# Kernel tuning notes

Hardware: AMD Instinct MI355X
Metric: run time of the kernel (lower is better)

## Reference

```python
import jax, jax.numpy as jnp
import numpy as np

B, T, D = 1, 2048, 3072
N, K, H = 16, 8, 256  # heads, kv heads, head dim
SOFT_CAP = 50.0
WINDOW = 1024
ROPE_BASE = 10000.0
ROPE_SCALE = 1.0
K_MASK = -2.3819763e+38
EPS = 1e-6


def rms_norm(x, scale=None):
    var = jnp.mean(jnp.square(x), axis=-1, keepdims=True)
    y = x * jax.lax.rsqrt(var + EPS)
    if scale is not None:
        y = y * (1.0 + scale)
    return y


def apply_rope(x, positions):
    # x: [B, T, n, H], positions: [B, T] int
    half = x.shape[-1] // 2
    fraction = 2.0 * jnp.arange(half, dtype=jnp.float32) / x.shape[-1]
    timescale = ROPE_BASE ** fraction  # [half]
    sinusoid = positions[..., None].astype(jnp.float32) / timescale  # [B,T,half]
    sinusoid = sinusoid[..., None, :] / ROPE_SCALE  # [B,T,1,half]
    sin, cos = jnp.sin(sinusoid), jnp.cos(sinusoid)
    first, second = jnp.split(x, 2, axis=-1)
    out = jnp.concatenate([first * cos - second * sin,
                           second * cos + first * sin], axis=-1)
    return out.astype(x.dtype)


def setup_inputs() -> dict:
    key = jax.random.key(0)
    ks = jax.random.split(key, 6)
    x = jax.random.normal(ks[0], (B, T, D), jnp.float32)
    segment_pos = jnp.broadcast_to(jnp.arange(T, dtype=jnp.int32), (B, T))
    attn_mask = jnp.broadcast_to(jnp.tril(jnp.ones((T, T), bool)), (B, T, T))
    w_q = jax.random.normal(ks[1], (N, D, H), jnp.float32) * 0.02
    w_kv = jax.random.normal(ks[2], (2, K, D, H), jnp.float32) * 0.02
    w_out = jax.random.normal(ks[3], (N, H, D), jnp.float32) * 0.02
    q_scale = jax.random.normal(ks[4], (H,), jnp.float32) * 0.1
    k_scale = jax.random.normal(ks[5], (H,), jnp.float32) * 0.1
    return {"x": x, "segment_pos": segment_pos, "attn_mask": attn_mask,
            "w_q": w_q, "w_kv": w_kv, "w_out": w_out,
            "q_scale": q_scale, "k_scale": k_scale}


def reference(x, segment_pos, attn_mask, w_q, w_kv, w_out, q_scale, k_scale):
    # Q projection + QK-RMSNorm + RoPE
    q = jnp.einsum('BTD,NDH->BTNH', x, w_q)
    q = rms_norm(q, q_scale)
    q = apply_rope(q, segment_pos)
    # fused KV projection
    kv = jnp.einsum('BSD,CKDH->CBSKH', x, w_kv)
    k_proj, v_proj = kv[0], kv[1]
    k_proj = rms_norm(k_proj, k_scale)
    v_proj = rms_norm(v_proj)  # value norm has no scale
    k_proj = apply_rope(k_proj, segment_pos)
    # GQA logits: q [B,T,K,G,H] x k [B,S,K,H]
    G = N // K
    qg = q.reshape(B, T, K, G, H)
    logits = jnp.einsum('BTKGH,BSKH->BTKGS', qg, k_proj).reshape(B, T, N, T)
    # logit soft-capping
    logits = jnp.tanh(logits / SOFT_CAP) * SOFT_CAP
    # sliding-window mask (cache_positions == segment_pos since cache is None)
    pos_q = segment_pos[:, :, None]
    pos_k = segment_pos[:, None, :]
    sliding = (pos_k > pos_q - WINDOW) & (pos_k < pos_q + WINDOW)  # [B,T,S]
    mask = attn_mask & sliding
    padded = jnp.where(mask[:, :, None, :], logits, K_MASK)
    probs = jax.nn.softmax(padded, axis=-1).astype(k_proj.dtype)
    enc = jnp.einsum('BTKGS,BSKH->BTKGH',
                     probs.reshape(B, T, K, G, T), v_proj).reshape(B, T, N, H)
    attn_output = jnp.einsum('BTNH,NHD->BTD', enc, w_out)
    return attn_output
```

## Files before the change

kernel.cpp:

```cpp
#include <hip/hip_runtime.h>
#include <math.h>

#define T_SEQ 2048
#define D_MODEL 3072
#define NQ 16
#define NKV 8
#define HD 256
#define NHEADS_TOT 32
#define QKV_COLS 8192
#define SOFT_CAP 50.0f
#define WINDOW 1024
#define K_MASK -2.3819763e38f

typedef __attribute__((ext_vector_type(8))) short bf16x8;
typedef __attribute__((ext_vector_type(4))) float f32x4;

__device__ __forceinline__ unsigned short f2bf(float f) {
    union { float f; unsigned u; } v; v.f = f;
    unsigned r = (v.u + 0x7fff + ((v.u >> 16) & 1)) >> 16;
    return (unsigned short)r;
}
__device__ __forceinline__ float bf2f(unsigned short u) {
    union { unsigned u; float f; } v; v.u = ((unsigned)u) << 16;
    return v.f;
}

__device__ __forceinline__ void gl_lds16(const unsigned short* g, unsigned short* l) {
    __builtin_amdgcn_global_load_lds(
        (const __attribute__((address_space(1))) void*)g,
        (__attribute__((address_space(3))) void*)l, 16, 0, 0);
}

__global__ __launch_bounds__(256) void k_convert(const float* __restrict__ src,
                                                 unsigned short* __restrict__ dst, int n4) {
    int i = blockIdx.x * 256 + threadIdx.x;
    if (i >= n4) return;
    float4 v = ((const float4*)src)[i];
    ushort4 o;
    o.x = f2bf(v.x); o.y = f2bf(v.y); o.z = f2bf(v.z); o.w = f2bf(v.w);
    ((ushort4*)dst)[i] = o;
}

__global__ __launch_bounds__(256) void k_transpose_bf16(const float* __restrict__ src,
                                                        unsigned short* __restrict__ dst,
                                                        int R, int C) {
    __shared__ float tile[32][33];
    int b = blockIdx.z;
    src += (size_t)b * R * C;
    dst += (size_t)b * R * C;
    int c0 = blockIdx.x * 32, r0 = blockIdx.y * 32;
    int tx = threadIdx.x, ty = threadIdx.y;
    #pragma unroll
    for (int i = ty; i < 32; i += 8)
        tile[i][tx] = src[(size_t)(r0 + i) * C + c0 + tx];
    __syncthreads();
    #pragma unroll
    for (int i = ty; i < 32; i += 8)
        dst[(size_t)(c0 + i) * R + r0 + tx] = f2bf(tile[tx][i]);
}

__global__ __launch_bounds__(256) void k_transpose_v(const unsigned short* __restrict__ src,
                                                     unsigned short* __restrict__ dst) {
    __shared__ unsigned short tile[32][34];
    int kk = blockIdx.z;
    src += (size_t)kk * T_SEQ * HD;
    dst += (size_t)kk * HD * T_SEQ;
    int h0 = blockIdx.x * 32, t0 = blockIdx.y * 32;
    int tx = threadIdx.x, ty = threadIdx.y;
    #pragma unroll
    for (int i = ty; i < 32; i += 8)
        tile[i][tx] = src[(size_t)(t0 + i) * HD + h0 + tx];
    __syncthreads();
    #pragma unroll
    for (int i = ty; i < 32; i += 8)
        dst[(size_t)(h0 + i) * T_SEQ + t0 + tx] = tile[tx][i];
}

__global__ __launch_bounds__(128) void k_trig(const int* __restrict__ spos,
                                              float2* __restrict__ tbl) {
    int t = blockIdx.x, hh = threadIdx.x;
    float fr = (float)hh * (1.0f / 128.0f);
    float ts = __expf(fr * 9.210340371976184f);
    float ang = (float)spos[t] / ts;
    float2 sc;
    sc.x = __sinf(ang);
    sc.y = __cosf(ang);
    tbl[(size_t)t * 128 + hh] = sc;
}

template <int OUT_BF16>
__global__ __launch_bounds__(256) void k_gemm_nt(const unsigned short* __restrict__ A,
                                                 const unsigned short* __restrict__ BT,
                                                 void* __restrict__ Cout,
                                                 int M, int N, int Kd) {
    __shared__ unsigned short As[128 * 64];
    __shared__ unsigned short Bs[128 * 64];
    const int tid = threadIdx.x;
    const int wave = tid >> 6, lane = tid & 63;
    const int col = lane & 15, quad = lane >> 4;
    const int wr = wave >> 1, wc = wave & 1;

    const int gx = M >> 7;
    int p = blockIdx.x;
    int xcd = p & 7, q = p >> 3;
    int i_t = q % gx, jj = q / gx;
    int j_t = jj * 8 + xcd;
    const int m0 = i_t * 128, n0 = j_t * 128;

    const int sub = wave & 1, isB = wave >> 1;
    const unsigned short* srcBase = isB ? (BT + (size_t)(n0 + sub * 64) * Kd)
                                        : (A + (size_t)(m0 + sub * 64) * Kd);
    unsigned short* ldsBase = (isB ? Bs : As) + sub * 64 * 64;
    const int lrow = lane >> 3, lchk = lane & 7;
    int soff[8];
    #pragma unroll
    for (int s = 0; s < 8; s++) {
        int r = s * 8 + lrow;
        soff[s] = r * Kd + ((lchk ^ (r & 7)) * 8);
    }

    f32x4 acc[4][4];
    #pragma unroll
    for (int i = 0; i < 4; i++)
        #pragma unroll
        for (int j = 0; j < 4; j++)
            acc[i][j] = (f32x4){0.f, 0.f, 0.f, 0.f};

    const int sw = col & 7;

    for (int k0 = 0; k0 < Kd; k0 += 64) {
        #pragma unroll
        for (int s = 0; s < 8; s++)
            gl_lds16(srcBase + soff[s] + k0, ldsBase + s * 512);
        __syncthreads();

        #pragma unroll
        for (int kk = 0; kk < 2; kk++) {
            bf16x8 af[4], bfr[4];
            const int chko = ((kk * 4 + quad) ^ sw) * 8;
            #pragma unroll
            for (int i = 0; i < 4; i++)
                af[i] = *(const bf16x8*)&As[(wr * 64 + i * 16 + col) * 64 + chko];
            #pragma unroll
            for (int j = 0; j < 4; j++)
                bfr[j] = *(const bf16x8*)&Bs[(wc * 64 + j * 16 + col) * 64 + chko];
            #pragma unroll
            for (int i = 0; i < 4; i++)
                #pragma unroll
                for (int j = 0; j < 4; j++)
                    acc[i][j] = __builtin_amdgcn_mfma_f32_16x16x32_bf16(af[i], bfr[j], acc[i][j], 0, 0, 0);
        }
        __syncthreads();
    }

    #pragma unroll
    for (int i = 0; i < 4; i++) {
        int row = m0 + wr * 64 + i * 16 + quad * 4;
        #pragma unroll
        for (int j = 0; j < 4; j++) {
            int c = n0 + wc * 64 + j * 16 + col;
            #pragma unroll
            for (int r = 0; r < 4; r++) {
                float v = acc[i][j][r];
                if (OUT_BF16)
                    ((unsigned short*)Cout)[(size_t)(row + r) * N + c] = f2bf(v);
                else
                    ((float*)Cout)[(size_t)(row + r) * N + c] = v;
            }
        }
    }
}

__global__ __launch_bounds__(256) void k_norm_rope(const unsigned short* __restrict__ qkv,
                                                   const float2* __restrict__ trig,
                                                   const float* __restrict__ qscale,
                                                   const float* __restrict__ kscale,
                                                   unsigned short* __restrict__ qh,
                                                   unsigned short* __restrict__ kh,
                                                   unsigned short* __restrict__ vh) {
    const int t = blockIdx.x, slot = blockIdx.y, h = threadIdx.x;
    float val = bf2f(qkv[(size_t)t * QKV_COLS + slot * HD + h]);
    float ss = val * val;
    #pragma unroll
    for (int m = 1; m < 64; m <<= 1) ss += __shfl_xor(ss, m, 64);
    __shared__ float wsum[4];
    __shared__ float ybuf[256];
    if ((h & 63) == 0) wsum[h >> 6] = ss;
    __syncthreads();
    float tot = wsum[0] + wsum[1] + wsum[2] + wsum[3];
    float y = val * rsqrtf(tot * (1.0f / 256.0f) + 1e-6f);
    if (slot < 16) y *= (1.0f + qscale[h]);
    else if (slot < 24) y *= (1.0f + kscale[h]);

    if (slot < 24) {
        ybuf[h] = y;
        __syncthreads();
        int hh = h & 127;
        float2 sc = trig[(size_t)t * 128 + hh];
        float sn = sc.x, cs = sc.y;
        float other = ybuf[(h < 128) ? (h + 128) : (h - 128)];
        float outv = (h < 128) ? (y * cs - other * sn) : (y * cs + other * sn);
        if (slot < 16)
            qh[((size_t)slot * T_SEQ + t) * HD + h] = f2bf(outv);
        else
            kh[((size_t)(slot - 16) * T_SEQ + t) * HD + h] = f2bf(outv);
    } else {
        vh[((size_t)(slot - 24) * T_SEQ + t) * HD + h] = f2bf(y);
    }
}

__global__ __launch_bounds__(256) void k_attn(const unsigned short* __restrict__ qh,
                                              const unsigned short* __restrict__ kh,
                                              const unsigned short* __restrict__ vT,
                                              unsigned short* __restrict__ enc) {
    __shared__ unsigned short Ks[32 * 256];
    __shared__ unsigned short Vs[256 * 32];
    __shared__ unsigned short Pl[4][16 * 40];

    const int tid = threadIdx.x;
    const int wave = tid >> 6, lane = tid & 63;
    const int col = lane & 15, quad = lane >> 4;
    const int kk = blockIdx.x;
    const int t0b = blockIdx.y * 32;
    const int headSel = wave & 1, rowSel = wave >> 1;
    const int n = kk * 2 + headSel;
    const int tw = t0b + rowSel * 16;

    const unsigned short* qp = qh + ((size_t)n * T_SEQ + tw) * HD;
    const unsigned short* kp = kh + (size_t)kk * T_SEQ * HD;
    const unsigned short* vp = vT + (size_t)kk * HD * T_SEQ;

    bf16x8 qf[8];
    #pragma unroll
    for (int c = 0; c < 8; c++)
        qf[c] = *(const bf16x8*)(qp + (size_t)col * HD + c * 32 + quad * 8);

    int preK[4], preV[4], ldsKo[4], ldsVo[4];
    #pragma unroll
    for (int i = 0; i < 4; i++) {
        int krow = 2 * (wave * 4 + i) + (lane >> 5);
        int kpos = lane & 31;
        preK[i] = krow * HD + ((kpos ^ (krow & 7)) * 8);
        ldsKo[i] = (wave * 4 + i) * 512;
        int vh2 = (wave * 4 + i) * 16 + (lane >> 2);
        int vpp = lane & 3;
        preV[i] = vh2 * T_SEQ + ((vpp ^ (vh2 & 3)) * 8);
        ldsVo[i] = (wave * 4 + i) * 512;
    }

    f32x4 o[16];
    #pragma unroll
    for (int h = 0; h < 16; h++) o[h] = (f32x4){0.f, 0.f, 0.f, 0.f};
    float lsum[4] = {0.f, 0.f, 0.f, 0.f};

    int s_begin = t0b - (WINDOW - 1);
    if (s_begin < 0) s_begin = 0;
    s_begin &= ~31;
    const int s_end = t0b + 32;

    for (int s0 = s_begin; s0 < s_end; s0 += 32) {
        #pragma unroll
        for (int i = 0; i < 4; i++)
            gl_lds16(kp + (size_t)s0 * HD + preK[i], &Ks[ldsKo[i]]);
        #pragma unroll
        for (int i = 0; i < 4; i++)
            gl_lds16(vp + (size_t)s0 + preV[i], &Vs[ldsVo[i]]);
        __syncthreads();

        f32x4 S0 = (f32x4){0.f, 0.f, 0.f, 0.f};
        f32x4 S1 = (f32x4){0.f, 0.f, 0.f, 0.f};
        #pragma unroll
        for (int c = 0; c < 8; c++) {
            bf16x8 kf = *(const bf16x8*)&Ks[(size_t)col * HD + (((c * 4 + quad) ^ (col & 7)) * 8)];
            S0 = __builtin_amdgcn_mfma_f32_16x16x32_bf16(qf[c], kf, S0, 0, 0, 0);
        }
        #pragma unroll
        for (int c = 0; c < 8; c++) {
            bf16x8 kf = *(const bf16x8*)&Ks[(size_t)(16 + col) * HD + (((c * 4 + quad) ^ (col & 7)) * 8)];
            S1 = __builtin_amdgcn_mfma_f32_16x16x32_bf16(qf[c], kf, S1, 0, 0, 0);
        }

        #pragma unroll
        for (int r = 0; r < 4; r++) {
            int t = tw + quad * 4 + r;
            int sA = s0 + col, sB = sA + 16;
            bool vA = (sA <= t) && (sA >= t - (WINDOW - 1));
            bool vB = (sB <= t) && (sB >= t - (WINDOW - 1));
            float eA = __expf(S0[r] * (2.0f / SOFT_CAP));
            float eB = __expf(S1[r] * (2.0f / SOFT_CAP));
            float rA = __builtin_amdgcn_rcpf(eA + 1.0f);
            float rB = __builtin_amdgcn_rcpf(eB + 1.0f);
            float pA = __expf(SOFT_CAP - 2.0f * SOFT_CAP * rA);
            float pB = __expf(SOFT_CAP - 2.0f * SOFT_CAP * rB);
            pA = vA ? pA : 0.0f;
            pB = vB ? pB : 0.0f;
            lsum[r] += pA + pB;
            Pl[wave][(quad * 4 + r) * 40 + col] = f2bf(pA);
            Pl[wave][(quad * 4 + r) * 40 + 16 + col] = f2bf(pB);
        }

        bf16x8 pf = *(const bf16x8*)&Pl[wave][col * 40 + quad * 8];

        #pragma unroll
        for (int ht = 0; ht < 16; ht++) {
            int h = ht * 16 + col;
            bf16x8 vf = *(const bf16x8*)&Vs[(size_t)h * 32 + ((quad ^ (h & 3)) * 8)];
            o[ht] = __builtin_amdgcn_mfma_f32_16x16x32_bf16(pf, vf, o[ht], 0, 0, 0);
        }
        __syncthreads();
    }

    #pragma unroll
    for (int r = 0; r < 4; r++) {
        #pragma unroll
        for (int m = 1; m < 16; m <<= 1)
            lsum[r] += __shfl_xor(lsum[r], m, 16);
        lsum[r] = 1.0f / lsum[r];
    }
    #pragma unroll
    for (int ht = 0; ht < 16; ht++) {
        #pragma unroll
        for (int r = 0; r < 4; r++) {
            int t = tw + quad * 4 + r;
            enc[(size_t)t * (NQ * HD) + n * HD + ht * 16 + col] = f2bf(o[ht][r] * lsum[r]);
        }
    }
}

extern "C" void kernel_launch(void* const* d_in, const int* in_sizes, int n_in,
                              void* d_out, int out_size, void* d_ws, size_t ws_size,
                              hipStream_t stream) {
    const float* x       = (const float*)d_in[0];
    const int*   spos    = (const int*)d_in[1];
    const float* w_q     = (const float*)d_in[3];
    const float* w_kv    = (const float*)d_in[4];
    const float* w_out   = (const float*)d_in[5];
    const float* q_scale = (const float*)d_in[6];
    const float* k_scale = (const float*)d_in[7];
    float* out = (float*)d_out;

    char* ws = (char*)d_ws;
    unsigned short* xb     = (unsigned short*)(ws + 0);
    unsigned short* vh     = (unsigned short*)(ws + 0);
    float2*         trig   = (float2*)(ws + 8388608);
    unsigned short* wT     = (unsigned short*)(ws + 12582912);
    unsigned short* wToutb = (unsigned short*)(ws + 12582912);
    unsigned short* encb   = (unsigned short*)(ws + 37748736);
    unsigned short* qkv    = (unsigned short*)(ws + 62914560);
    unsigned short* qh     = (unsigned short*)(ws + 96468992);
    unsigned short* kh     = (unsigned short*)(ws + 113246208);
    unsigned short* vT     = (unsigned short*)(ws + 121634816);

    k_convert<<<dim3((T_SEQ * D_MODEL / 4 + 255) / 256), dim3(256), 0, stream>>>(
        x, xb, T_SEQ * D_MODEL / 4);
    k_transpose_bf16<<<dim3(HD / 32, D_MODEL / 32, NQ), dim3(32, 8), 0, stream>>>(
        w_q, wT, D_MODEL, HD);
    k_transpose_bf16<<<dim3(HD / 32, D_MODEL / 32, 16), dim3(32, 8), 0, stream>>>(
        w_kv, wT + (size_t)4096 * D_MODEL, D_MODEL, HD);
    k_gemm_nt<1><<<dim3((T_SEQ / 128) * (QKV_COLS / 128)), dim3(256), 0, stream>>>(
        xb, wT, qkv, T_SEQ, QKV_COLS, D_MODEL);
    k_trig<<<dim3(T_SEQ), dim3(128), 0, stream>>>(spos, trig);
    k_transpose_bf16<<<dim3(D_MODEL / 32, 4096 / 32, 1), dim3(32, 8), 0, stream>>>(
        w_out, wToutb, 4096, D_MODEL);
    k_norm_rope<<<dim3(T_SEQ, NHEADS_TOT), dim3(256), 0, stream>>>(
        qkv, trig, q_scale, k_scale, qh, kh, vh);
    k_transpose_v<<<dim3(HD / 32, T_SEQ / 32, NKV), dim3(32, 8), 0, stream>>>(vh, vT);
    k_attn<<<dim3(NKV, T_SEQ / 32), dim3(256), 0, stream>>>(qh, kh, vT, encb);
    k_gemm_nt<0><<<dim3((T_SEQ / 128) * (D_MODEL / 128)), dim3(256), 0, stream>>>(
        encb, wToutb, out, T_SEQ, D_MODEL, NQ * HD);
}
```

Measured before the change: 550.2 us.

## Use 128x64-tile GEMM for output projection and batch four heads per norm-rope block

```diff
diff --git a/kernel.cpp b/kernel.cpp
--- a/kernel.cpp
+++ b/kernel.cpp
@@ -171,6 +171,88 @@
     }
 }
 
+__global__ __launch_bounds__(256) void k_gemm2(const unsigned short* __restrict__ A,
+                                               const unsigned short* __restrict__ BT,
+                                               float* __restrict__ C,
+                                               int M, int N, int Kd) {
+    __shared__ unsigned short As[128 * 64];
+    __shared__ unsigned short Bs[64 * 64];
+    const int tid = threadIdx.x;
+    const int wave = tid >> 6, lane = tid & 63;
+    const int col = lane & 15, quad = lane >> 4;
+
+    const int gx = M >> 7;
+    int p = blockIdx.x;
+    int xcd = p & 7, q = p >> 3;
+    int i_t = q % gx, jj = q / gx;
+    int j_t = jj * 8 + xcd;
+    const int m0 = i_t * 128, n0 = j_t * 64;
+
+    const int lrow = lane >> 3, lchk = lane & 7;
+    int soffA[4], soffB[2];
+    #pragma unroll
+    for (int s = 0; s < 4; s++) {
+        int r = (wave * 4 + s) * 8 + lrow;
+        soffA[s] = r * Kd + ((lchk ^ (r & 7)) * 8);
+    }
+    #pragma unroll
+    for (int s = 0; s < 2; s++) {
+        int r = (wave * 2 + s) * 8 + lrow;
+        soffB[s] = r * Kd + ((lchk ^ (r & 7)) * 8);
+    }
+    const unsigned short* Ab = A + (size_t)m0 * Kd;
+    const unsigned short* Bb = BT + (size_t)n0 * Kd;
+
+    f32x4 acc[2][4];
+    #pragma unroll
+    for (int i = 0; i < 2; i++)
+        #pragma unroll
+        for (int j = 0; j < 4; j++)
+            acc[i][j] = (f32x4){0.f, 0.f, 0.f, 0.f};
+
+    const int sw = col & 7;
+
+    for (int k0 = 0; k0 < Kd; k0 += 64) {
+        #pragma unroll
+        for (int s = 0; s < 4; s++)
+            gl_lds16(Ab + soffA[s] + k0, &As[(wave * 4 + s) * 512]);
+        #pragma unroll
+        for (int s = 0; s < 2; s++)
+            gl_lds16(Bb + soffB[s] + k0, &Bs[(wave * 2 + s) * 512]);
+        __syncthreads();
+
+        #pragma unroll
+        for (int kk = 0; kk < 2; kk++) {
+            const int chko = ((kk * 4 + quad) ^ sw) * 8;
+            bf16x8 af[2], bfr[4];
+            #pragma unroll
+            for (int i = 0; i < 2; i++)
+                af[i] = *(const bf16x8*)&As[(wave * 32 + i * 16 + col) * 64 + chko];
+            #pragma unroll
+            for (int j = 0; j < 4; j++)
+                bfr[j] = *(const bf16x8*)&Bs[(j * 16 + col) * 64 + chko];
+            #pragma unroll
+            for (int i = 0; i < 2; i++)
+                #pragma unroll
+                for (int j = 0; j < 4; j++)
+                    acc[i][j] = __builtin_amdgcn_mfma_f32_16x16x32_bf16(af[i], bfr[j], acc[i][j], 0, 0, 0);
+        }
+        __syncthreads();
+    }
+
+    #pragma unroll
+    for (int i = 0; i < 2; i++) {
+        int row = m0 + wave * 32 + i * 16 + quad * 4;
+        #pragma unroll
+        for (int j = 0; j < 4; j++) {
+            int c = n0 + j * 16 + col;
+            #pragma unroll
+            for (int r = 0; r < 4; r++)
+                C[(size_t)(row + r) * N + c] = acc[i][j][r];
+        }
+    }
+}
+
 __global__ __launch_bounds__(256) void k_norm_rope(const unsigned short* __restrict__ qkv,
                                                    const float2* __restrict__ trig,
                                                    const float* __restrict__ qscale,
@@ -178,35 +260,56 @@
                                                    unsigned short* __restrict__ qh,
                                                    unsigned short* __restrict__ kh,
                                                    unsigned short* __restrict__ vh) {
-    const int t = blockIdx.x, slot = blockIdx.y, h = threadIdx.x;
-    float val = bf2f(qkv[(size_t)t * QKV_COLS + slot * HD + h]);
-    float ss = val * val;
-    #pragma unroll
-    for (int m = 1; m < 64; m <<= 1) ss += __shfl_xor(ss, m, 64);
-    __shared__ float wsum[4];
-    __shared__ float ybuf[256];
-    if ((h & 63) == 0) wsum[h >> 6] = ss;
+    const int t = blockIdx.x, y = blockIdx.y, h = threadIdx.x;
+    __shared__ float wsum[4][4];
+    __shared__ float ybuf[3][256];
+
+    float val[4];
+    #pragma unroll
+    for (int g = 0; g < 4; g++)
+        val[g] = bf2f(qkv[(size_t)t * QKV_COLS + (y + g * 8) * HD + h]);
+
+    float ssg[4];
+    #pragma unroll
+    for (int g = 0; g < 4; g++) {
+        float ss = val[g] * val[g];
+        #pragma unroll
+        for (int m = 1; m < 64; m <<= 1) ss += __shfl_xor(ss, m, 64);
+        ssg[g] = ss;
+    }
+    if ((h & 63) == 0) {
+        #pragma unroll
+        for (int g = 0; g < 4; g++) wsum[g][h >> 6] = ssg[g];
+    }
     __syncthreads();
-    float tot = wsum[0] + wsum[1] + wsum[2] + wsum[3];
-    float y = val * rsqrtf(tot * (1.0f / 256.0f) + 1e-6f);
-    if (slot < 16) y *= (1.0f + qscale[h]);
-    else if (slot < 24) y *= (1.0f + kscale[h]);
-
-    if (slot < 24) {
-        ybuf[h] = y;
-        __syncthreads();
-        int hh = h & 127;
-        float2 sc = trig[(size_t)t * 128 + hh];
-        float sn = sc.x, cs = sc.y;
-        float other = ybuf[(h < 128) ? (h + 128) : (h - 128)];
-        float outv = (h < 128) ? (y * cs - other * sn) : (y * cs + other * sn);
+
+    float2 sc = trig[(size_t)t * 128 + (h & 127)];
+    float qs = 1.0f + qscale[h], ks = 1.0f + kscale[h];
+
+    float yv[4];
+    #pragma unroll
+    for (int g = 0; g < 4; g++) {
+        float tot = wsum[g][0] + wsum[g][1] + wsum[g][2] + wsum[g][3];
+        float yy = val[g] * rsqrtf(tot * (1.0f / 256.0f) + 1e-6f);
+        if (g < 2) yy *= qs;
+        else if (g == 2) yy *= ks;
+        yv[g] = yy;
+        if (g < 3) ybuf[g][h] = yy;
+    }
+    __syncthreads();
+
+    #pragma unroll
+    for (int g = 0; g < 3; g++) {
+        float other = ybuf[g][(h < 128) ? (h + 128) : (h - 128)];
+        float outv = (h < 128) ? (yv[g] * sc.y - other * sc.x)
+                               : (yv[g] * sc.y + other * sc.x);
+        int slot = y + g * 8;
         if (slot < 16)
             qh[((size_t)slot * T_SEQ + t) * HD + h] = f2bf(outv);
         else
             kh[((size_t)(slot - 16) * T_SEQ + t) * HD + h] = f2bf(outv);
-    } else {
-        vh[((size_t)(slot - 24) * T_SEQ + t) * HD + h] = f2bf(y);
-    }
+    }
+    vh[((size_t)y * T_SEQ + t) * HD + h] = f2bf(yv[3]);
 }
 
 __global__ __launch_bounds__(256) void k_attn(const unsigned short* __restrict__ qh,
@@ -362,10 +465,10 @@
     k_trig<<<dim3(T_SEQ), dim3(128), 0, stream>>>(spos, trig);
     k_transpose_bf16<<<dim3(D_MODEL / 32, 4096 / 32, 1), dim3(32, 8), 0, stream>>>(
         w_out, wToutb, 4096, D_MODEL);
-    k_norm_rope<<<dim3(T_SEQ, NHEADS_TOT), dim3(256), 0, stream>>>(
+    k_norm_rope<<<dim3(T_SEQ, 8), dim3(256), 0, stream>>>(
         qkv, trig, q_scale, k_scale, qh, kh, vh);
     k_transpose_v<<<dim3(HD / 32, T_SEQ / 32, NKV), dim3(32, 8), 0, stream>>>(vh, vT);
     k_attn<<<dim3(NKV, T_SEQ / 32), dim3(256), 0, stream>>>(qh, kh, vT, encb);
-    k_gemm_nt<0><<<dim3((T_SEQ / 128) * (D_MODEL / 128)), dim3(256), 0, stream>>>(
+    k_gemm2<<<dim3((T_SEQ / 128) * (D_MODEL / 64)), dim3(256), 0, stream>>>(
         encb, wToutb, out, T_SEQ, D_MODEL, NQ * HD);
 }
```

After: 517.9 us. 1.06x faster.
